# Performance work log

Measured on AMD Instinct MI355X. Metric: run time of the kernel, lower is better.

## Reference

```python
import jax, jax.numpy as jnp
import numpy as np

H = 16
NEG = -1e10

def setup_inputs() -> dict:
    key = jax.random.key(0)
    ks = jax.random.split(key, 12)
    B, S, D = 2, 2048, 1024
    sc = 1.0 / np.sqrt(D)
    inp = {
        'q': jax.random.normal(ks[0], (B, S, D), jnp.float32),
        'k': jax.random.normal(ks[1], (B, S, D), jnp.float32),
        'v': jax.random.normal(ks[2], (B, S, D), jnp.float32),
        'Wq': jax.random.normal(ks[3], (D, D), jnp.float32) * sc,
        'bq': jax.random.normal(ks[4], (D,), jnp.float32) * 0.02,
        'Wk': jax.random.normal(ks[5], (D, D), jnp.float32) * sc,
        'bk': jax.random.normal(ks[6], (D,), jnp.float32) * 0.02,
        'Wv': jax.random.normal(ks[7], (D, D), jnp.float32) * sc,
        'bv': jax.random.normal(ks[8], (D,), jnp.float32) * 0.02,
        'Wo': jax.random.normal(ks[9], (D, D), jnp.float32) * sc,
        'bo': jax.random.normal(ks[10], (D,), jnp.float32) * 0.02,
        'mask': jax.random.randint(ks[11], (B, S, S), 0, 2, jnp.int32),
    }
    return inp

def reference(q, k, v, Wq, bq, Wk, bk, Wv, bv, Wo, bo, mask):
    B, S, D = q.shape
    dk = D // H
    # projections (torch Linear: x @ W.T + b), split heads -> [B,H,S,dk]
    qh = (q @ Wq.T + bq).reshape(B, S, H, dk).transpose(0, 2, 1, 3)
    kh = (k @ Wk.T + bk).reshape(B, S, H, dk).transpose(0, 2, 1, 3)
    vh = (v @ Wv.T + bv).reshape(B, S, H, dk).transpose(0, 2, 1, 3)
    # scaled dot-product scores [B,H,Sq,Sk]
    scores = jnp.einsum('bhqd,bhkd->bhqk', qh, kh) / jnp.sqrt(jnp.float32(dk))
    scores = jnp.where(mask[:, None, :, :] == 0, jnp.float32(NEG), scores)
    attn = jax.nn.softmax(scores, axis=-1)  # dropout in eval mode = identity
    ctx = jnp.einsum('bhqk,bhkd->bhqd', attn, vh)
    concat = ctx.transpose(0, 2, 1, 3).reshape(B, S, D)
    return concat @ Wo.T + bo
```

## Files before the change

kernel.cpp:

```cpp
#include <hip/hip_runtime.h>
#include <hip/hip_bf16.h>
#include <stdint.h>

typedef __bf16 bf16;
typedef __bf16 bf16x2 __attribute__((ext_vector_type(2)));
typedef __bf16 bf16x4 __attribute__((ext_vector_type(4)));
typedef __bf16 bf16x8 __attribute__((ext_vector_type(8)));
typedef float f32x4 __attribute__((ext_vector_type(4)));
typedef float f32x16 __attribute__((ext_vector_type(16)));
typedef unsigned int u32;
typedef u32 u32x4 __attribute__((ext_vector_type(4)));
typedef unsigned long long u64;

#define MFMA16(a, b, c) __builtin_amdgcn_mfma_f32_16x16x32_bf16((a), (b), (c), 0, 0, 0)
#define MFMA32(a, b, c) __builtin_amdgcn_mfma_f32_32x32x16_bf16((a), (b), (c), 0, 0, 0)

constexpr int Bc = 2, Sc = 2048, Dc = 1024, Hc = 16, DKc = 64;
constexpr int Mc = Bc * Sc;
constexpr int MW = Sc / 64;
#define QSCALE 0.1803368801111731f

__device__ __forceinline__ u32 pk2(float a, float b) {
  bf16x2 t; t[0] = (bf16)a; t[1] = (bf16)b;
  return __builtin_bit_cast(u32, t);
}

__device__ __forceinline__ void gl_lds16(const void* g, void* l) {
  __builtin_amdgcn_global_load_lds((const __attribute__((address_space(1))) void*)g,
                                   (__attribute__((address_space(3))) void*)l, 16, 0, 0);
}

__global__ __launch_bounds__(256) void convw_kernel(
    const float* __restrict__ wq, const float* __restrict__ wk,
    const float* __restrict__ wv, const float* __restrict__ wo,
    bf16* __restrict__ dq, bf16* __restrict__ dk2, bf16* __restrict__ dv, bf16* __restrict__ dwo) {
  const int a = blockIdx.y;
  const float* src = a == 0 ? wq : a == 1 ? wk : a == 2 ? wv : wo;
  bf16* dst = a == 0 ? dq : a == 1 ? dk2 : a == 2 ? dv : dwo;
  const float sc = a == 0 ? QSCALE : 1.0f;
  const size_t i = ((size_t)blockIdx.x * 256 + threadIdx.x) * 8;
  f32x4 x0 = *(const f32x4*)&src[i];
  f32x4 x1 = *(const f32x4*)&src[i + 4];
  bf16x8 o;
#pragma unroll
  for (int j = 0; j < 4; ++j) { o[j] = (bf16)(x0[j] * sc); o[4 + j] = (bf16)(x1[j] * sc); }
  *(bf16x8*)&dst[i] = o;
}

__global__ __launch_bounds__(256) void packmask_kernel(const int* __restrict__ mask,
                                                       u64* __restrict__ mbT, int nwords) {
  const int lane = threadIdx.x & 63;
  const int wid = (blockIdx.x * blockDim.x + threadIdx.x) >> 6;
  const int nw = (gridDim.x * blockDim.x) >> 6;
  for (int i = wid; i < nwords; i += nw) {
    int v = mask[(size_t)i * 64 + lane];
    u64 bits = __ballot(v != 0);
    if (lane == 0) {
      const int kw = i & (MW - 1), bq = i >> 5;
      const int b = bq >> 11, q = bq & (Sc - 1);
      mbT[((size_t)(b * MW + kw)) * Sc + q] = bits;
    }
  }
}

__global__ __launch_bounds__(256, 2) void gemm_qkv_kernel(
    const float* __restrict__ q, const float* __restrict__ k, const float* __restrict__ v,
    const bf16* __restrict__ wq, const bf16* __restrict__ wk, const bf16* __restrict__ wv,
    const float* __restrict__ bq, const float* __restrict__ bk, const float* __restrict__ bv,
    bf16* __restrict__ qh, bf16* __restrict__ kh, bf16* __restrict__ vt) {
  __shared__ float As[128 * 64];
  __shared__ bf16 Bs[128 * 64];
  const int d = blockIdx.x;
  const int xcd = d & 7, idx = d >> 3;
  const int proj = idx >> 5, w = idx & 31;
  const int n0 = (w & 7) * 128;
  const int m0 = (xcd * 4 + (w >> 3)) * 128;
  const float* Af = proj == 0 ? q : proj == 1 ? k : v;
  const bf16* Bw = proj == 0 ? wq : proj == 1 ? wk : wv;
  const float* bias = proj == 0 ? bq : proj == 1 ? bk : bv;

  const int t = threadIdx.x, lane = t & 63, wv4 = t >> 6;
  const int c = lane & 15, g = lane >> 4;
  const int wr = wv4 >> 1, wc = wv4 & 1;

  f32x4 acc[4][4];
#pragma unroll
  for (int i = 0; i < 4; ++i)
#pragma unroll
    for (int j = 0; j < 4; ++j) acc[i][j] = (f32x4){0.f, 0.f, 0.f, 0.f};

  const int arow_l = lane >> 4;
  const int aslot_l = lane & 15;
  const int brow_l = lane >> 3;
  const int bslot_l = (lane & 7) ^ brow_l;

  for (int k0 = 0; k0 < Dc; k0 += 64) {
#pragma unroll
    for (int u = 0; u < 8; ++u) {
      const int ch = wv4 * 8 + u;
      const int row = ch * 4 + arow_l;
      const int slot = aslot_l ^ (row & 7);
      gl_lds16(&Af[(size_t)(m0 + row) * Dc + k0 + slot * 4], &As[ch * 256]);
    }
#pragma unroll
    for (int u = 0; u < 4; ++u) {
      const int ch = wv4 * 4 + u;
      const int row = ch * 8 + brow_l;
      gl_lds16(&Bw[(size_t)(n0 + row) * Dc + k0 + bslot_l * 8], &Bs[ch * 512]);
    }
    __syncthreads();
#pragma unroll
    for (int ks = 0; ks < 2; ++ks) {
      bf16x8 af[4], bfr[4];
#pragma unroll
      for (int mt = 0; mt < 4; ++mt) {
        const int row = wr * 64 + mt * 16 + c;
        const int s0 = (8 * ks + 2 * g) ^ (c & 7);
        const int s1 = (8 * ks + 2 * g + 1) ^ (c & 7);
        f32x4 lo = *(const f32x4*)&As[row * 64 + s0 * 4];
        f32x4 hi2 = *(const f32x4*)&As[row * 64 + s1 * 4];
#pragma unroll
        for (int j = 0; j < 4; ++j) { af[mt][j] = (bf16)lo[j]; af[mt][4 + j] = (bf16)hi2[j]; }
      }
#pragma unroll
      for (int nt = 0; nt < 4; ++nt) {
        const int row = wc * 64 + nt * 16 + c;
        const int sl = (4 * ks + g) ^ (c & 7);
        bfr[nt] = *(const bf16x8*)&Bs[row * 64 + sl * 8];
      }
#pragma unroll
      for (int mt = 0; mt < 4; ++mt)
#pragma unroll
        for (int nt = 0; nt < 4; ++nt) acc[mt][nt] = MFMA16(af[mt], bfr[nt], acc[mt][nt]);
    }
    __syncthreads();
  }

  const float bsc = proj == 0 ? QSCALE : 1.0f;
  const int colb = n0 + wc * 64 + c;
  const int mrowb = m0 + wr * 64 + 4 * g;
#pragma unroll
  for (int mt = 0; mt < 4; ++mt) {
#pragma unroll
    for (int nt = 0; nt < 4; ++nt) {
      const int col = colb + nt * 16;
      const int mrow = mrowb + mt * 16;
      const float bb = bias[col] * bsc;
      f32x4 a = acc[mt][nt];
      if (proj == 0) {
#pragma unroll
        for (int r = 0; r < 4; ++r) qh[(size_t)(mrow + r) * Dc + col] = (bf16)(a[r] + bb);
      } else if (proj == 1) {
        const int hh = col >> 6, dd = col & 63;
#pragma unroll
        for (int r = 0; r < 4; ++r) {
          const int mr = mrow + r;
          kh[((size_t)((mr >> 11) * Hc + hh) * Sc + (mr & (Sc - 1))) * DKc + dd] = (bf16)(a[r] + bb);
        }
      } else {
        const int batch = mrow >> 11, s = mrow & (Sc - 1);
        const int hh = col >> 6, dd = col & 63;
        bf16x4 pkv;
#pragma unroll
        for (int r = 0; r < 4; ++r) pkv[r] = (bf16)(a[r] + bb);
        *(bf16x4*)&vt[((size_t)((batch * Hc + hh) * DKc + dd)) * Sc + s] = pkv;
      }
    }
  }
}

__global__ __launch_bounds__(256, 2) void gemm_o_kernel(const bf16* __restrict__ ctxp,
                                                        const bf16* __restrict__ wo,
                                                        const float* __restrict__ bo,
                                                        float* __restrict__ outp) {
  __shared__ bf16 As[128 * 64];
  __shared__ bf16 Bs[64 * 64];
  const int d = blockIdx.x;
  const int xcd = d & 7, idx = d >> 3;
  const int n0 = (idx & 15) * 64;
  const int m0 = (xcd * 4 + (idx >> 4)) * 128;

  const int t = threadIdx.x, lane = t & 63, wv4 = t >> 6;
  const int c = lane & 15, g = lane >> 4;
  const int brow_l = lane >> 3;
  const int bslot_l = (lane & 7) ^ brow_l;

  f32x4 acc[2][4];
#pragma unroll
  for (int i = 0; i < 2; ++i)
#pragma unroll
    for (int j = 0; j < 4; ++j) acc[i][j] = (f32x4){0.f, 0.f, 0.f, 0.f};

  for (int k0 = 0; k0 < Dc; k0 += 64) {
#pragma unroll
    for (int u = 0; u < 4; ++u) {
      const int ch = wv4 * 4 + u;
      const int row = ch * 8 + brow_l;
      gl_lds16(&ctxp[(size_t)(m0 + row) * Dc + k0 + bslot_l * 8], &As[ch * 512]);
    }
    {
      const int ch = wv4;
      const int row = ch * 8 + brow_l;
      gl_lds16(&wo[(size_t)(n0 + row) * Dc + k0 + bslot_l * 8], &Bs[ch * 512]);
      const int ch2 = 4 + wv4;
      const int row2 = ch2 * 8 + brow_l;
      gl_lds16(&wo[(size_t)(n0 + row2) * Dc + k0 + bslot_l * 8], &Bs[ch2 * 512]);
    }
    __syncthreads();
#pragma unroll
    for (int ks = 0; ks < 2; ++ks) {
      bf16x8 af[2], bfr[4];
#pragma unroll
      for (int mt = 0; mt < 2; ++mt) {
        const int row = wv4 * 32 + mt * 16 + c;
        const int sl = (4 * ks + g) ^ (c & 7);
        af[mt] = *(const bf16x8*)&As[row * 64 + sl * 8];
      }
#pragma unroll
      for (int nt = 0; nt < 4; ++nt) {
        const int row = nt * 16 + c;
        const int sl = (4 * ks + g) ^ (c & 7);
        bfr[nt] = *(const bf16x8*)&Bs[row * 64 + sl * 8];
      }
#pragma unroll
      for (int mt = 0; mt < 2; ++mt)
#pragma unroll
        for (int nt = 0; nt < 4; ++nt) acc[mt][nt] = MFMA16(af[mt], bfr[nt], acc[mt][nt]);
    }
    __syncthreads();
  }

  const int colb = n0 + c;
  const int mrowb = m0 + wv4 * 32 + 4 * g;
#pragma unroll
  for (int mt = 0; mt < 2; ++mt)
#pragma unroll
    for (int nt = 0; nt < 4; ++nt) {
      const int col = colb + nt * 16;
      const int mrow = mrowb + mt * 16;
      const float bb = bo[col];
      f32x4 a = acc[mt][nt];
#pragma unroll
      for (int r = 0; r < 4; ++r) outp[(size_t)(mrow + r) * Dc + col] = a[r] + bb;
    }
}

template <int SPLITS>
__global__ __launch_bounds__(256, 2) void attn_kernel(const bf16* __restrict__ qh,
                                                      const bf16* __restrict__ kh,
                                                      const bf16* __restrict__ vt,
                                                      const u64* __restrict__ mbT,
                                                      bf16* __restrict__ ctx,
                                                      float* __restrict__ opart,
                                                      float2* __restrict__ ml) {
  __shared__ bf16 Ks[2][128 * 64];
  __shared__ bf16 Vs[2][64 * 128];
  const int d = blockIdx.x;
  const int xcd = d & 7, idx = d >> 3;
  int bh, qt, half;
  if constexpr (SPLITS == 2) {
    bh = xcd * 4 + (idx >> 5);
    const int sub = idx & 31;
    qt = sub >> 1; half = sub & 1;
  } else {
    bh = xcd * 4 + (idx >> 4);
    qt = idx & 15; half = 0;
  }
  const int b = bh >> 4, h = bh & 15;
  const int lane = threadIdx.x & 63, wv4 = threadIdx.x >> 6;
  const int ql = lane & 31, hi = lane >> 5;
  const int qrow = qt * 128 + wv4 * 32 + ql;

  const bf16* Qp = qh + (size_t)(b * Sc + qrow) * Dc + h * DKc;
  const bf16* Kp = kh + (size_t)(b * Hc + h) * Sc * DKc;
  const bf16* Vp = vt + (size_t)(b * Hc + h) * DKc * Sc;
  const u64* mbp = mbT + (size_t)b * MW * Sc;

  const int k0 = half * (Sc / SPLITS);
  constexpr int NIT = (Sc / SPLITS) / 128;

  const int srow = lane >> 3, sslot = lane & 7;
  const int vrow = lane >> 4, vslot = lane & 15;
  auto stage = [&](int buf, int kt) {
#pragma unroll
    for (int u = 0; u < 4; ++u) {
      const int ch = wv4 * 4 + u;
      const int r = ch * 8 + srow;
      gl_lds16(&Kp[(size_t)(kt + r) * DKc + (size_t)((sslot ^ (r & 7)) * 8)], &Ks[buf][ch * 512]);
    }
#pragma unroll
    for (int u = 0; u < 4; ++u) {
      const int ch = wv4 * 4 + u;
      const int r = ch * 4 + vrow;
      gl_lds16(&Vp[(size_t)r * Sc + kt + (size_t)((vslot ^ (r & 7)) * 8)], &Vs[buf][ch * 512]);
    }
  };

  bf16x8 qf[4];
#pragma unroll
  for (int ka = 0; ka < 4; ++ka) qf[ka] = *(const bf16x8*)&Qp[16 * ka + 8 * hi];

  bf16x8 ones8;
#pragma unroll
  for (int j = 0; j < 8; ++j) ones8[j] = (bf16)1.0f;

  f32x16 oacc[2], lacc;
#pragma unroll
  for (int i = 0; i < 2; ++i)
#pragma unroll
    for (int r = 0; r < 16; ++r) oacc[i][r] = 0.f;
#pragma unroll
  for (int r = 0; r < 16; ++r) lacc[r] = 0.f;

  stage(0, k0);
  u64 w0 = mbp[(size_t)((k0 >> 6) + 0) * Sc + qrow];
  u64 w1 = mbp[(size_t)((k0 >> 6) + 1) * Sc + qrow];
  asm volatile("s_waitcnt vmcnt(0)" ::: "memory");
  __builtin_amdgcn_s_barrier();
  __builtin_amdgcn_sched_barrier(0);

  for (int it = 0; it < NIT; ++it) {
    const int kt = k0 + it * 128;
    const int buf = it & 1;
    const int ktn = (it + 1 < NIT) ? kt + 128 : kt;
    stage(buf ^ 1, ktn);
    const u64 w0n = mbp[(size_t)((ktn >> 6) + 0) * Sc + qrow];
    const u64 w1n = mbp[(size_t)((ktn >> 6) + 1) * Sc + qrow];

#pragma unroll
    for (int hh = 0; hh < 2; ++hh) {
      const u64 w = hh ? w1 : w0;

      f32x16 st[2];
#pragma unroll
      for (int tt = 0; tt < 2; ++tt) {
        const int row = 64 * hh + 32 * tt + ql;
        const bf16* kbase = &Ks[buf][row * 64];
        f32x16 z;
#pragma unroll
        for (int r = 0; r < 16; ++r) z[r] = 0.f;
        __builtin_amdgcn_s_setprio(1);
#pragma unroll
        for (int ka = 0; ka < 4; ++ka) {
          bf16x8 kf = *(const bf16x8*)&kbase[((2 * ka + hi) ^ (row & 7)) * 8];
          z = MFMA32(kf, qf[ka], z);
        }
        __builtin_amdgcn_s_setprio(0);
        st[tt] = z;
      }

      const u32 wt0 = (u32)(w >> (4 * hi));
      const u32 wt1 = (u32)(w >> (32 + 4 * hi));
#pragma unroll
      for (int tt = 0; tt < 2; ++tt) {
        const u32 wt = tt ? wt1 : wt0;
#pragma unroll
        for (int r = 0; r < 16; ++r) {
          const int bit = (r & 3) + 8 * (r >> 2);
          const float p = exp2f((float)st[tt][r]);
          st[tt][r] = ((wt >> bit) & 1u) ? p : 0.f;
        }
      }

      u32x4 pb[4];
#pragma unroll
      for (int ks = 0; ks < 4; ++ks) {
        const int tt = ks >> 1, e = ks & 1;
#pragma unroll
        for (int w2 = 0; w2 < 4; ++w2)
          pb[ks][w2] = pk2((float)st[tt][8 * e + 2 * w2], (float)st[tt][8 * e + 2 * w2 + 1]);
      }

      __builtin_amdgcn_s_setprio(1);
#pragma unroll
      for (int ks = 0; ks < 4; ++ks)
        lacc = MFMA32(ones8, __builtin_bit_cast(bf16x8, pb[ks]), lacc);
#pragma unroll
      for (int dt = 0; dt < 2; ++dt) {
        const int row = 32 * dt + ql;
        const bf16* vbase = &Vs[buf][row * 128];
#pragma unroll
        for (int ks = 0; ks < 4; ++ks) {
          const int slot0 = (8 * hh + 2 * ks) ^ (row & 7);
          bf16x4 vlo = *(const bf16x4*)&vbase[slot0 * 8 + 4 * hi];
          bf16x4 vhi = *(const bf16x4*)&vbase[(slot0 ^ 1) * 8 + 4 * hi];
          bf16x8 vf;
#pragma unroll
          for (int j = 0; j < 4; ++j) { vf[j] = vlo[j]; vf[4 + j] = vhi[j]; }
          oacc[dt] = MFMA32(vf, __builtin_bit_cast(bf16x8, pb[ks]), oacc[dt]);
        }
      }
      __builtin_amdgcn_s_setprio(0);
    }

    asm volatile("s_waitcnt vmcnt(0)" ::: "memory");
    __builtin_amdgcn_s_barrier();
    __builtin_amdgcn_sched_barrier(0);
    w0 = w0n; w1 = w1n;
  }

  const float lsum = lacc[0];
  if constexpr (SPLITS == 2) {
    float* opr = opart + ((size_t)(half * 32 + bh) * Sc + qrow) * 64;
#pragma unroll
    for (int dt = 0; dt < 2; ++dt)
#pragma unroll
      for (int i = 0; i < 4; ++i) {
        f32x4 o4;
#pragma unroll
        for (int rr = 0; rr < 4; ++rr) o4[rr] = oacc[dt][4 * i + rr];
        *(f32x4*)&opr[32 * dt + 8 * i + 4 * hi] = o4;
      }
    if (hi == 0) {
      float2 v2; v2.x = 0.f; v2.y = lsum;
      ml[(size_t)(half * 32 + bh) * Sc + qrow] = v2;
    }
  } else {
    const float rinv = 1.f / fmaxf(lsum, 1e-35f);
    bf16* cp = ctx + (size_t)(b * Sc + qrow) * Dc + h * DKc;
#pragma unroll
    for (int dt = 0; dt < 2; ++dt)
#pragma unroll
      for (int i = 0; i < 4; ++i) {
        bf16x4 o4;
#pragma unroll
        for (int rr = 0; rr < 4; ++rr) o4[rr] = (bf16)(oacc[dt][4 * i + rr] * rinv);
        *(bf16x4*)&cp[32 * dt + 8 * i + 4 * hi] = o4;
      }
  }
}

__global__ __launch_bounds__(256) void combine_kernel(const float* __restrict__ op,
                                                      const float2* __restrict__ ml,
                                                      bf16* __restrict__ ctx) {
  const int wv = threadIdx.x >> 6, lane = threadIdx.x & 63;
  const size_t row = (size_t)blockIdx.x * 4 + wv;
  const int bh = (int)(row >> 11), q = (int)(row & 2047);
  const int b = bh >> 4, h = bh & 15;
  const float2 ml0 = ml[row], ml1 = ml[65536 + row];
  const float o0 = op[row * 64 + lane];
  const float o1 = op[(size_t)65536 * 64 + row * 64 + lane];
  const float m = fmaxf(ml0.x, ml1.x);
  const float a0 = exp2f(ml0.x - m), a1 = exp2f(ml1.x - m);
  const float l = fmaxf(a0 * ml0.y + a1 * ml1.y, 1e-35f);
  const float o = (a0 * o0 + a1 * o1) / l;
  ctx[((size_t)(b * Sc + q)) * Dc + h * DKc + lane] = (bf16)o;
}

extern "C" void kernel_launch(void* const* d_in, const int* in_sizes, int n_in,
                              void* d_out, int out_size, void* d_ws, size_t ws_size,
                              hipStream_t stream) {
  (void)in_sizes; (void)n_in; (void)out_size;
  const float* q  = (const float*)d_in[0];
  const float* k  = (const float*)d_in[1];
  const float* v  = (const float*)d_in[2];
  const float* Wq = (const float*)d_in[3];
  const float* bq = (const float*)d_in[4];
  const float* Wk = (const float*)d_in[5];
  const float* bk = (const float*)d_in[6];
  const float* Wv = (const float*)d_in[7];
  const float* bv = (const float*)d_in[8];
  const float* Wo = (const float*)d_in[9];
  const float* bo = (const float*)d_in[10];
  const int* mask = (const int*)d_in[11];

  char* ws = (char*)d_ws;
  size_t off = 0;
  auto take = [&](size_t bytes) -> void* {
    void* p = ws + off;
    off += (bytes + 255) & ~(size_t)255;
    return p;
  };
  bf16* qh  = (bf16*)take((size_t)Mc * Dc * 2);
  bf16* kh  = (bf16*)take((size_t)Mc * Dc * 2);
  bf16* vt  = (bf16*)take((size_t)Mc * Dc * 2);
  bf16* ctx = (bf16*)take((size_t)Mc * Dc * 2);
  u64* mbits = (u64*)take((size_t)Bc * Sc * MW * 8);
  bf16* wqb = (bf16*)take((size_t)Dc * Dc * 2);
  bf16* wkb = (bf16*)take((size_t)Dc * Dc * 2);
  bf16* wvb = (bf16*)take((size_t)Dc * Dc * 2);
  bf16* wob = (bf16*)take((size_t)Dc * Dc * 2);
  float* opart = (float*)take((size_t)2 * 32 * Sc * 64 * 4);
  float2* mlb = (float2*)take((size_t)2 * 32 * Sc * 8);
  const bool split2 = off <= ws_size;

  convw_kernel<<<dim3(512, 4), 256, 0, stream>>>(Wq, Wk, Wv, Wo, wqb, wkb, wvb, wob);
  packmask_kernel<<<512, 256, 0, stream>>>(mask, mbits, Bc * Sc * Sc / 64);
  gemm_qkv_kernel<<<768, 256, 0, stream>>>(q, k, v, wqb, wkb, wvb, bq, bk, bv, qh, kh, vt);
  if (split2) {
    attn_kernel<2><<<1024, 256, 0, stream>>>(qh, kh, vt, mbits, ctx, opart, mlb);
    combine_kernel<<<16384, 256, 0, stream>>>(opart, mlb, ctx);
  } else {
    attn_kernel<1><<<512, 256, 0, stream>>>(qh, kh, vt, mbits, ctx, opart, mlb);
  }
  gemm_o_kernel<<<512, 256, 0, stream>>>(ctx, wob, bo, (float*)d_out);
}
```

Baseline: 177.6 us.

## Halve attention K tile, permute V layout for single 128-bit LDS reads, raise occupancy

The V projection epilogue now writes the transposed V with a permutation inside each 16-element group of the sequence dimension. This lets the attention kernel load each V MFMA operand with a single 16-byte LDS read instead of two 8-byte reads plus a repack. The attention key tile shrinks from 128 to 64, which halves the LDS buffers and raises launch bounds to 4 blocks per CU for more occupancy. The kernel also switches to the raw hardware exp2 builtin. The trade-off is twice as many loop iterations and barriers, and more register pressure at the higher occupancy target.

```diff
diff --git a/kernel.cpp b/kernel.cpp
--- a/kernel.cpp
+++ b/kernel.cpp
@@ -159,11 +159,12 @@
         }
       } else {
         const int batch = mrow >> 11, s = mrow & (Sc - 1);
+        const int s2 = (s & ~15) | ((s & 4) << 1) | ((s & 8) >> 1);
         const int hh = col >> 6, dd = col & 63;
         bf16x4 pkv;
 #pragma unroll
         for (int r = 0; r < 4; ++r) pkv[r] = (bf16)(a[r] + bb);
-        *(bf16x4*)&vt[((size_t)((batch * Hc + hh) * DKc + dd)) * Sc + s] = pkv;
+        *(bf16x4*)&vt[((size_t)((batch * Hc + hh) * DKc + dd)) * Sc + s2] = pkv;
       }
     }
   }
@@ -246,15 +247,15 @@
 }
 
 template <int SPLITS>
-__global__ __launch_bounds__(256, 2) void attn_kernel(const bf16* __restrict__ qh,
+__global__ __launch_bounds__(256, 4) void attn_kernel(const bf16* __restrict__ qh,
                                                       const bf16* __restrict__ kh,
                                                       const bf16* __restrict__ vt,
                                                       const u64* __restrict__ mbT,
                                                       bf16* __restrict__ ctx,
                                                       float* __restrict__ opart,
                                                       float2* __restrict__ ml) {
-  __shared__ bf16 Ks[2][128 * 64];
-  __shared__ bf16 Vs[2][64 * 128];
+  __shared__ bf16 Ks[2][64 * 64];
+  __shared__ bf16 Vs[2][64 * 64];
   const int d = blockIdx.x;
   const int xcd = d & 7, idx = d >> 3;
   int bh, qt, half;
@@ -277,22 +278,21 @@
   const u64* mbp = mbT + (size_t)b * MW * Sc;
 
   const int k0 = half * (Sc / SPLITS);
-  constexpr int NIT = (Sc / SPLITS) / 128;
+  constexpr int NIT = (Sc / SPLITS) / 64;
 
   const int srow = lane >> 3, sslot = lane & 7;
-  const int vrow = lane >> 4, vslot = lane & 15;
   auto stage = [&](int buf, int kt) {
 #pragma unroll
-    for (int u = 0; u < 4; ++u) {
-      const int ch = wv4 * 4 + u;
+    for (int u = 0; u < 2; ++u) {
+      const int ch = wv4 * 2 + u;
       const int r = ch * 8 + srow;
       gl_lds16(&Kp[(size_t)(kt + r) * DKc + (size_t)((sslot ^ (r & 7)) * 8)], &Ks[buf][ch * 512]);
     }
 #pragma unroll
-    for (int u = 0; u < 4; ++u) {
-      const int ch = wv4 * 4 + u;
-      const int r = ch * 4 + vrow;
-      gl_lds16(&Vp[(size_t)r * Sc + kt + (size_t)((vslot ^ (r & 7)) * 8)], &Vs[buf][ch * 512]);
+    for (int u = 0; u < 2; ++u) {
+      const int ch = wv4 * 2 + u;
+      const int r = ch * 8 + srow;
+      gl_lds16(&Vp[(size_t)r * Sc + kt + (size_t)((sslot ^ (r & 7)) * 8)], &Vs[buf][ch * 512]);
     }
   };
 
@@ -313,90 +313,78 @@
   for (int r = 0; r < 16; ++r) lacc[r] = 0.f;
 
   stage(0, k0);
-  u64 w0 = mbp[(size_t)((k0 >> 6) + 0) * Sc + qrow];
-  u64 w1 = mbp[(size_t)((k0 >> 6) + 1) * Sc + qrow];
+  u64 w = mbp[(size_t)(k0 >> 6) * Sc + qrow];
   asm volatile("s_waitcnt vmcnt(0)" ::: "memory");
   __builtin_amdgcn_s_barrier();
   __builtin_amdgcn_sched_barrier(0);
 
   for (int it = 0; it < NIT; ++it) {
-    const int kt = k0 + it * 128;
+    const int kt = k0 + it * 64;
     const int buf = it & 1;
-    const int ktn = (it + 1 < NIT) ? kt + 128 : kt;
+    const int ktn = (it + 1 < NIT) ? kt + 64 : kt;
     stage(buf ^ 1, ktn);
-    const u64 w0n = mbp[(size_t)((ktn >> 6) + 0) * Sc + qrow];
-    const u64 w1n = mbp[(size_t)((ktn >> 6) + 1) * Sc + qrow];
-
-#pragma unroll
-    for (int hh = 0; hh < 2; ++hh) {
-      const u64 w = hh ? w1 : w0;
-
-      f32x16 st[2];
-#pragma unroll
-      for (int tt = 0; tt < 2; ++tt) {
-        const int row = 64 * hh + 32 * tt + ql;
-        const bf16* kbase = &Ks[buf][row * 64];
-        f32x16 z;
-#pragma unroll
-        for (int r = 0; r < 16; ++r) z[r] = 0.f;
-        __builtin_amdgcn_s_setprio(1);
-#pragma unroll
-        for (int ka = 0; ka < 4; ++ka) {
-          bf16x8 kf = *(const bf16x8*)&kbase[((2 * ka + hi) ^ (row & 7)) * 8];
-          z = MFMA32(kf, qf[ka], z);
-        }
-        __builtin_amdgcn_s_setprio(0);
-        st[tt] = z;
-      }
-
-      const u32 wt0 = (u32)(w >> (4 * hi));
-      const u32 wt1 = (u32)(w >> (32 + 4 * hi));
-#pragma unroll
-      for (int tt = 0; tt < 2; ++tt) {
-        const u32 wt = tt ? wt1 : wt0;
-#pragma unroll
-        for (int r = 0; r < 16; ++r) {
-          const int bit = (r & 3) + 8 * (r >> 2);
-          const float p = exp2f((float)st[tt][r]);
-          st[tt][r] = ((wt >> bit) & 1u) ? p : 0.f;
-        }
-      }
-
-      u32x4 pb[4];
+    const u64 wn = mbp[(size_t)(ktn >> 6) * Sc + qrow];
+
+    f32x16 st[2];
+#pragma unroll
+    for (int tt = 0; tt < 2; ++tt) {
+      const int row = 32 * tt + ql;
+      const bf16* kbase = &Ks[buf][row * 64];
+      f32x16 z;
+#pragma unroll
+      for (int r = 0; r < 16; ++r) z[r] = 0.f;
+      __builtin_amdgcn_s_setprio(1);
+#pragma unroll
+      for (int ka = 0; ka < 4; ++ka) {
+        bf16x8 kf = *(const bf16x8*)&kbase[((2 * ka + hi) ^ (row & 7)) * 8];
+        z = MFMA32(kf, qf[ka], z);
+      }
+      __builtin_amdgcn_s_setprio(0);
+      st[tt] = z;
+    }
+
+    const u32 wt0 = (u32)(w >> (4 * hi));
+    const u32 wt1 = (u32)(w >> (32 + 4 * hi));
+#pragma unroll
+    for (int tt = 0; tt < 2; ++tt) {
+      const u32 wt = tt ? wt1 : wt0;
+#pragma unroll
+      for (int r = 0; r < 16; ++r) {
+        const int bit = (r & 3) + 8 * (r >> 2);
+        const float p = __builtin_amdgcn_exp2f((float)st[tt][r]);
+        st[tt][r] = ((wt >> bit) & 1u) ? p : 0.f;
+      }
+    }
+
+    u32x4 pb[4];
+#pragma unroll
+    for (int ks = 0; ks < 4; ++ks) {
+      const int tt = ks >> 1, e = ks & 1;
+#pragma unroll
+      for (int w2 = 0; w2 < 4; ++w2)
+        pb[ks][w2] = pk2((float)st[tt][8 * e + 2 * w2], (float)st[tt][8 * e + 2 * w2 + 1]);
+    }
+
+    __builtin_amdgcn_s_setprio(1);
+#pragma unroll
+    for (int ks = 0; ks < 4; ++ks)
+      lacc = MFMA32(ones8, __builtin_bit_cast(bf16x8, pb[ks]), lacc);
+#pragma unroll
+    for (int dt = 0; dt < 2; ++dt) {
+      const int row = 32 * dt + ql;
+      const bf16* vbase = &Vs[buf][row * 64];
 #pragma unroll
       for (int ks = 0; ks < 4; ++ks) {
-        const int tt = ks >> 1, e = ks & 1;
-#pragma unroll
-        for (int w2 = 0; w2 < 4; ++w2)
-          pb[ks][w2] = pk2((float)st[tt][8 * e + 2 * w2], (float)st[tt][8 * e + 2 * w2 + 1]);
-      }
-
-      __builtin_amdgcn_s_setprio(1);
-#pragma unroll
-      for (int ks = 0; ks < 4; ++ks)
-        lacc = MFMA32(ones8, __builtin_bit_cast(bf16x8, pb[ks]), lacc);
-#pragma unroll
-      for (int dt = 0; dt < 2; ++dt) {
-        const int row = 32 * dt + ql;
-        const bf16* vbase = &Vs[buf][row * 128];
-#pragma unroll
-        for (int ks = 0; ks < 4; ++ks) {
-          const int slot0 = (8 * hh + 2 * ks) ^ (row & 7);
-          bf16x4 vlo = *(const bf16x4*)&vbase[slot0 * 8 + 4 * hi];
-          bf16x4 vhi = *(const bf16x4*)&vbase[(slot0 ^ 1) * 8 + 4 * hi];
-          bf16x8 vf;
-#pragma unroll
-          for (int j = 0; j < 4; ++j) { vf[j] = vlo[j]; vf[4 + j] = vhi[j]; }
-          oacc[dt] = MFMA32(vf, __builtin_bit_cast(bf16x8, pb[ks]), oacc[dt]);
-        }
-      }
-      __builtin_amdgcn_s_setprio(0);
-    }
+        bf16x8 vf = *(const bf16x8*)&vbase[((2 * ks + hi) ^ (row & 7)) * 8];
+        oacc[dt] = MFMA32(vf, __builtin_bit_cast(bf16x8, pb[ks]), oacc[dt]);
+      }
+    }
+    __builtin_amdgcn_s_setprio(0);
 
     asm volatile("s_waitcnt vmcnt(0)" ::: "memory");
     __builtin_amdgcn_s_barrier();
     __builtin_amdgcn_sched_barrier(0);
-    w0 = w0n; w1 = w1n;
+    w = wn;
   }
 
   const float lsum = lacc[0];
```

Result: faster. 170.0 us (-4.3%).
